# Kernel tuning notes

Measured on AMD Instinct MI355X. Metric: run time of the kernel, lower is better.

The kernel has to match this reference:

```python
import jax, jax.numpy as jnp
import numpy as np

B, M, E, H, A = 32, 512, 256, 8, 64


def setup_inputs() -> dict:
    key = jax.random.key(0)
    k0, k1, k2, k3, k4 = jax.random.split(key, 5)
    s = 1.0 / np.sqrt(E)
    x = jax.random.normal(k0, (B, M, E), dtype=jnp.float32)
    Wq = jax.random.normal(k1, (E, H * A), dtype=jnp.float32) * s
    Wk = jax.random.normal(k2, (E, H * A), dtype=jnp.float32) * s
    Wv = jax.random.normal(k3, (E, H * A), dtype=jnp.float32) * s
    Wr = jax.random.normal(k4, (E, A), dtype=jnp.float32) * s
    return {"x": x, "Wq": Wq, "Wk": Wk, "Wv": Wv, "Wr": Wr}


def reference(x, Wq, Wk, Wv, Wr):
    # Faithful to the original: (B, M, H*A) tensors are view()'d directly to
    # (H, B, M, A) / (H, B, A, M) without any transpose — this mixes batch
    # into the head axis exactly as the torch code does.
    q = (x @ Wq).reshape(H, B, M, A)   # query view
    k = (x @ Wk).reshape(H, B, A, M)   # keys viewed pre-transposed
    v = (x @ Wv).reshape(H, B, M, A)
    scores = jnp.einsum('hbma,hban->hbmn', q, k)      # (H, B, M, M)
    att = jax.nn.softmax(scores, axis=-1)
    out = jnp.einsum('hbmn,hbna->hbma', att, v)       # (H, B, M, A)
    out = out.mean(axis=0)                            # head-mean -> (B, M, A)
    return jax.nn.relu(out + x @ Wr)
```

## Files before the change

### kernel.cpp

```cpp
#include <hip/hip_runtime.h>
#include <math.h>


typedef _Float16 f16;
typedef _Float16 f16x2 __attribute__((ext_vector_type(2)));
typedef _Float16 f16x4 __attribute__((ext_vector_type(4)));
typedef _Float16 f16x8 __attribute__((ext_vector_type(8)));
typedef float    f32x4 __attribute__((ext_vector_type(4)));

typedef __attribute__((address_space(1))) const void* gas_t;
typedef __attribute__((address_space(3))) void* las_t;

__device__ __forceinline__ void gload16(const void* g, void* l) {
  __builtin_amdgcn_global_load_lds((gas_t)g, (las_t)l, 16, 0, 0);
}

__global__ __launch_bounds__(256) void k_cast(const float* __restrict__ in,
                                              f16* __restrict__ out, int n4) {
  int i = blockIdx.x * 256 + threadIdx.x;
  if (i < n4) {
    f32x4 v = reinterpret_cast<const f32x4*>(in)[i];
    f16x4 h;
    h[0] = (f16)v[0]; h[1] = (f16)v[1]; h[2] = (f16)v[2]; h[3] = (f16)v[3];
    reinterpret_cast<f16x4*>(out)[i] = h;
  }
}

__global__ __launch_bounds__(256) void k_transpose_w(const float* __restrict__ Wq,
                                                     const float* __restrict__ Wk,
                                                     const float* __restrict__ Wv,
                                                     const float* __restrict__ Wr,
                                                     f16* __restrict__ Wt,
                                                     f16* __restrict__ Wrt) {
  __shared__ f16 tile[64][68];
  int b = blockIdx.x;
  const float* src; f16* dst; int r0, c0, Cin;
  if (b < 96) {
    int ws = b >> 5, rem = b & 31;
    src = (ws == 0) ? Wq : (ws == 1) ? Wk : Wv;
    dst = Wt + ws * 512 * 256;
    Cin = 512; r0 = (rem >> 3) * 64; c0 = (rem & 7) * 64;
  } else {
    src = Wr; dst = Wrt; Cin = 64; r0 = (b - 96) * 64; c0 = 0;
  }
  int t = threadIdx.x;
#pragma unroll
  for (int u = 0; u < 8; ++u) {
    int e = u * 256 + t;
    int r = e >> 5, c = (e & 31) << 1;
    const float* p = src + (long)(r0 + r) * Cin + (c0 + c);
    f16x2 v; v[0] = (f16)p[0]; v[1] = (f16)p[1];
    *reinterpret_cast<f16x2*>(&tile[r][c]) = v;
  }
  __syncthreads();
#pragma unroll
  for (int u = 0; u < 16; ++u) {
    int f = u * 256 + t;
    int cc = f >> 6, rr = f & 63;
    dst[(long)(c0 + cc) * 256 + (r0 + rr)] = tile[rr][cc];
  }
}

template <int BN, bool F32OUT>
__global__ __launch_bounds__(256, 3) void k_gemm(const f16* __restrict__ Xh,
                                                 const f16* __restrict__ Wt,
                                                 f16* __restrict__ outH,
                                                 float* __restrict__ outF, int N) {
  __shared__ f16 Ash[128 * 64];
  __shared__ f16 Bsh[BN * 64];
  constexpr int NT = BN / 32;
  int t = threadIdx.x;
  int w = t >> 6, l = t & 63;
  int lrow = l & 15, lg = l >> 4;
  int wm = w >> 1, wn = w & 1;
  int rb = blockIdx.x * 128, cb = blockIdx.y * BN;

  f32x4 acc[4][NT] = {};

  for (int kt = 0; kt < 4; ++kt) {
    int kb = kt * 64;
    __syncthreads();
#pragma unroll
    for (int i = 0; i < 4; ++i) {
      int slot = i * 256 + t;
      int row = slot >> 3, pblk = slot & 7;
      int blk = pblk ^ (row & 7);
      gload16(Xh + (long)(rb + row) * 256 + kb + blk * 8, Ash + slot * 8);
    }
#pragma unroll
    for (int i = 0; i < BN / 32; ++i) {
      int slot = i * 256 + t;
      int row = slot >> 3, pblk = slot & 7;
      int blk = pblk ^ (row & 7);
      gload16(Wt + (long)(cb + row) * 256 + kb + blk * 8, Bsh + slot * 8);
    }
    __syncthreads();

    f16x8 af[4][2];
#pragma unroll
    for (int mi = 0; mi < 4; ++mi)
#pragma unroll
      for (int ks = 0; ks < 2; ++ks) {
        int r = 64 * wm + 16 * mi + lrow;
        af[mi][ks] = *reinterpret_cast<const f16x8*>(
            Ash + r * 64 + (((4 * ks + lg) ^ (lrow & 7)) * 8));
      }
#pragma unroll
    for (int nt = 0; nt < NT; ++nt) {
      int rB = (BN / 2) * wn + 16 * nt + lrow;
      f16x8 b0 = *reinterpret_cast<const f16x8*>(Bsh + rB * 64 + ((lg ^ (lrow & 7)) * 8));
      f16x8 b1 = *reinterpret_cast<const f16x8*>(Bsh + rB * 64 + (((4 + lg) ^ (lrow & 7)) * 8));
#pragma unroll
      for (int mi = 0; mi < 4; ++mi) {
        acc[mi][nt] = __builtin_amdgcn_mfma_f32_16x16x32_f16(af[mi][0], b0, acc[mi][nt], 0, 0, 0);
        acc[mi][nt] = __builtin_amdgcn_mfma_f32_16x16x32_f16(af[mi][1], b1, acc[mi][nt], 0, 0, 0);
      }
    }
  }
#pragma unroll
  for (int mi = 0; mi < 4; ++mi)
#pragma unroll
    for (int nt = 0; nt < NT; ++nt)
#pragma unroll
      for (int r = 0; r < 4; ++r) {
        int row = rb + 64 * wm + 16 * mi + 4 * (l >> 4) + r;
        int col = cb + (BN / 2) * wn + 16 * nt + lrow;
        float v = acc[mi][nt][r];
        if constexpr (F32OUT) {
          outF[(long)row * N + col] = v;
        } else {
          long idx = ((long)(col >> 9) << 23) + (long)row * 512 + (col & 511);
          outH[idx] = (f16)v;
        }
      }
}

__global__ __launch_bounds__(256, 4) void k_attn(const f16* __restrict__ Qh,
                                                 const f16* __restrict__ Kn,
                                                 const f16* __restrict__ Vn,
                                                 f16* __restrict__ Of) {
  __shared__ f16 Ksh[64 * 64];
  __shared__ f16 Vsh[64 * 64];
  __shared__ f16 Psh[4][32][72];
  int g = blockIdx.x, mb = blockIdx.y;
  int t = threadIdx.x, w = t >> 6, l = t & 63;
  int lrow = l & 15, lg = l >> 4, lk8 = lg * 8;
  long gp = (long)g * 32768;
  const f16* Qg = Qh + gp;
  const f16* Kg = Kn + gp;
  const f16* Vg = Vn + gp;
  f16* Og = Of + gp;
  int m0 = mb * 128 + w * 32;

  int sa = t >> 3;
  int so = (t & 7) * 8;

  f16x8 qf[2][2];
#pragma unroll
  for (int mi = 0; mi < 2; ++mi)
#pragma unroll
    for (int ks = 0; ks < 2; ++ks)
      qf[mi][ks] = *reinterpret_cast<const f16x8*>(Qg + (long)(m0 + 16 * mi + lrow) * 64 + 32 * ks + lk8);

  f32x4 accO[2][4] = {};
  float Mx[2] = {-INFINITY, -INFINITY}, Ls[2] = {0.f, 0.f};

  auto write_stage = [&](f16x8 kr0, f16x8 kr1, f16x8 vr0, f16x8 vr1) {
#pragma unroll
    for (int s = 0; s < 2; ++s) {
      f16x8 kr = s ? kr1 : kr0;
      int a = s * 32 + sa;
      int ab = a >> 3;
#pragma unroll
      for (int j = 0; j < 8; ++j) {
        int n = so + j;
        Ksh[n * 64 + ((ab ^ (n >> 3)) * 8) + (a & 7)] = kr[j];
      }
      f16x8 vr = s ? vr1 : vr0;
      int n2 = s * 32 + sa;
      int nb = n2 >> 3;
#pragma unroll
      for (int j = 0; j < 8; ++j) {
        int aa = so + j;
        Vsh[aa * 64 + ((nb ^ (aa >> 3)) * 8) + (n2 & 7)] = vr[j];
      }
    }
  };

  {
    f16x8 k0 = *reinterpret_cast<const f16x8*>(Kg + (long)(0 * 32 + sa) * 512 + so);
    f16x8 k1 = *reinterpret_cast<const f16x8*>(Kg + (long)(1 * 32 + sa) * 512 + so);
    f16x8 v0 = *reinterpret_cast<const f16x8*>(Vg + (long)(0 * 32 + sa) * 64 + so);
    f16x8 v1 = *reinterpret_cast<const f16x8*>(Vg + (long)(32 + sa) * 64 + so);
    write_stage(k0, k1, v0, v1);
  }
  __syncthreads();

  for (int c = 0; c < 8; ++c) {
    f16x8 kn0, kn1, vn0, vn1;
    if (c < 7) {
      int cn = c + 1;
      kn0 = *reinterpret_cast<const f16x8*>(Kg + (long)(0 * 32 + sa) * 512 + cn * 64 + so);
      kn1 = *reinterpret_cast<const f16x8*>(Kg + (long)(1 * 32 + sa) * 512 + cn * 64 + so);
      vn0 = *reinterpret_cast<const f16x8*>(Vg + (long)(cn * 64 + sa) * 64 + so);
      vn1 = *reinterpret_cast<const f16x8*>(Vg + (long)(cn * 64 + 32 + sa) * 64 + so);
    }

    f32x4 St[2][4] = {};
#pragma unroll
    for (int nt = 0; nt < 4; ++nt) {
      int n = 16 * nt + lrow, nb = n >> 3;
      f16x8 ka = *reinterpret_cast<const f16x8*>(Ksh + n * 64 + ((lg ^ nb) * 8));
      f16x8 kb = *reinterpret_cast<const f16x8*>(Ksh + n * 64 + (((4 + lg) ^ nb) * 8));
#pragma unroll
      for (int mi = 0; mi < 2; ++mi) {
        St[mi][nt] = __builtin_amdgcn_mfma_f32_16x16x32_f16(ka, qf[mi][0], St[mi][nt], 0, 0, 0);
        St[mi][nt] = __builtin_amdgcn_mfma_f32_16x16x32_f16(kb, qf[mi][1], St[mi][nt], 0, 0, 0);
      }
    }

    float scb[2][4];
#pragma unroll
    for (int mi = 0; mi < 2; ++mi) {
      float tm = St[mi][0][0];
#pragma unroll
      for (int nt = 0; nt < 4; ++nt)
#pragma unroll
        for (int r = 0; r < 4; ++r) tm = fmaxf(tm, St[mi][nt][r]);
      tm = fmaxf(tm, __shfl_xor(tm, 16));
      tm = fmaxf(tm, __shfl_xor(tm, 32));
      float nm = fmaxf(Mx[mi], tm);
      float sc = __expf(Mx[mi] - nm);
      Mx[mi] = nm;
      float ps = 0.f;
#pragma unroll
      for (int nt = 0; nt < 4; ++nt)
#pragma unroll
        for (int r = 0; r < 4; ++r) {
          float p = __expf(St[mi][nt][r] - nm);
          St[mi][nt][r] = p;
          ps += p;
        }
      ps += __shfl_xor(ps, 16);
      ps += __shfl_xor(ps, 32);
      Ls[mi] = Ls[mi] * sc + ps;
#pragma unroll
      for (int nt = 0; nt < 4; ++nt) {
        f16x4 p4;
        p4[0] = (f16)St[mi][nt][0]; p4[1] = (f16)St[mi][nt][1];
        p4[2] = (f16)St[mi][nt][2]; p4[3] = (f16)St[mi][nt][3];
        *reinterpret_cast<f16x4*>(&Psh[w][16 * mi + lrow][16 * nt + 4 * lg]) = p4;
      }
#pragma unroll
      for (int r = 0; r < 4; ++r) scb[mi][r] = __shfl(sc, 20 * lg + r);
    }
#pragma unroll
    for (int mi = 0; mi < 2; ++mi)
#pragma unroll
      for (int at = 0; at < 4; ++at)
#pragma unroll
        for (int r = 0; r < 4; ++r) accO[mi][at][r] *= scb[mi][r];

#pragma unroll
    for (int ks = 0; ks < 2; ++ks) {
      f16x8 pa[2];
#pragma unroll
      for (int mi = 0; mi < 2; ++mi)
        pa[mi] = *reinterpret_cast<const f16x8*>(&Psh[w][16 * mi + lrow][32 * ks + lk8]);
#pragma unroll
      for (int at = 0; at < 4; ++at) {
        int a = 16 * at + lrow, ab = a >> 3;
        f16x8 vb = *reinterpret_cast<const f16x8*>(Vsh + a * 64 + (((4 * ks + lg) ^ ab) * 8));
#pragma unroll
        for (int mi = 0; mi < 2; ++mi)
          accO[mi][at] = __builtin_amdgcn_mfma_f32_16x16x32_f16(pa[mi], vb, accO[mi][at], 0, 0, 0);
      }
    }

    __syncthreads();
    if (c < 7) write_stage(kn0, kn1, vn0, vn1);
    __syncthreads();
  }

#pragma unroll
  for (int mi = 0; mi < 2; ++mi) {
    float inv = 1.f / Ls[mi];
    float invb[4];
#pragma unroll
    for (int r = 0; r < 4; ++r) invb[r] = __shfl(inv, 20 * lg + r);
#pragma unroll
    for (int r = 0; r < 4; ++r) {
      int row = m0 + 16 * mi + 4 * lg + r;
#pragma unroll
      for (int at = 0; at < 4; ++at)
        Og[(long)row * 64 + 16 * at + lrow] = (f16)(accO[mi][at][r] * invb[r]);
    }
  }
}

__global__ __launch_bounds__(256) void k_finalize(const f16* __restrict__ Of,
                                                  const float* __restrict__ Rf,
                                                  float* __restrict__ out) {
  int i = blockIdx.x * 256 + threadIdx.x;
  f32x4 s = {};
#pragma unroll
  for (int h = 0; h < 8; ++h) {
    f16x4 o = reinterpret_cast<const f16x4*>(Of + (long)h * 1048576)[i];
#pragma unroll
    for (int j = 0; j < 4; ++j) s[j] += (float)o[j];
  }
  f32x4 r = reinterpret_cast<const f32x4*>(Rf)[i];
  f32x4 v = s * 0.125f + r;
#pragma unroll
  for (int j = 0; j < 4; ++j) v[j] = v[j] > 0.f ? v[j] : 0.f;
  reinterpret_cast<f32x4*>(out)[i] = v;
}

extern "C" void kernel_launch(void* const* d_in, const int* in_sizes, int n_in,
                              void* d_out, int out_size, void* d_ws, size_t ws_size,
                              hipStream_t stream) {
  const float* x  = (const float*)d_in[0];
  const float* Wq = (const float*)d_in[1];
  const float* Wk = (const float*)d_in[2];
  const float* Wv = (const float*)d_in[3];
  const float* Wr = (const float*)d_in[4];
  float* out = (float*)d_out;
  char* w = (char*)d_ws;

  f16*   Xh   = (f16*)(w + 0);
  f16*   Wt   = (f16*)(w + 8388608);
  f16*   Wrt  = (f16*)(w + 9175040);
  f16*   QKV  = (f16*)(w + 9207808);
  f16*   Qh   = QKV;
  f16*   Kn   = (f16*)(w + 25985024);
  f16*   Vn   = (f16*)(w + 42762240);
  float* Rf   = (float*)(w + 59539456);
  f16*   Of   = (f16*)(w + 63733760);

  k_cast<<<4096, 256, 0, stream>>>(x, Xh, 1048576);
  k_transpose_w<<<100, 256, 0, stream>>>(Wq, Wk, Wv, Wr, Wt, Wrt);

  k_gemm<128, false><<<dim3(128, 12), 256, 0, stream>>>(Xh, Wt, QKV, nullptr, 512);
  k_gemm<64, true><<<dim3(128, 1), 256, 0, stream>>>(Xh, Wrt, nullptr, Rf, 64);

  k_attn<<<dim3(256, 4), 256, 0, stream>>>(Qh, Kn, Vn, Of);
  k_finalize<<<1024, 256, 0, stream>>>(Of, Rf, out);
}
```

Before: 155.1 us.

## Pre-transpose K and V in global memory and drop LDS staging in attention

Two new transpose kernels rewrite K (64x512 per group) and V (512x64 per group) into transposed layouts ahead of attention. The attention kernel then reads MFMA operands straight from global memory and no longer uses LDS staging, the per-chunk barriers or the software prefetch. It also remaps block indices so the four row-blocks of a group run close together for L2 reuse, and raises wave priority around the MFMA sections. In exchange it adds two extra kernel launches and a full read and write of K and V, and the direct global loads may expose memory latency.

```diff
diff --git a/kernel.cpp b/kernel.cpp
--- a/kernel.cpp
+++ b/kernel.cpp
@@ -61,6 +61,31 @@
   }
 }
 
+__global__ __launch_bounds__(256) void k_transpose(const f16* __restrict__ in,
+                                                   f16* __restrict__ out,
+                                                   int R_, int C_) {
+  __shared__ f16 tile[64][68];
+  int g = blockIdx.x;
+  long gb = (long)g * R_ * C_;
+  int r0 = blockIdx.y * 64, c0 = blockIdx.z * 64;
+  int t = threadIdx.x;
+#pragma unroll
+  for (int u = 0; u < 8; ++u) {
+    int e = u * 256 + t;
+    int r = e >> 5, c = (e & 31) << 1;
+    const f16* p = in + gb + (long)(r0 + r) * C_ + (c0 + c);
+    f16x2 v; v[0] = p[0]; v[1] = p[1];
+    *reinterpret_cast<f16x2*>(&tile[r][c]) = v;
+  }
+  __syncthreads();
+#pragma unroll
+  for (int u = 0; u < 16; ++u) {
+    int f = u * 256 + t;
+    int cc = f >> 6, rr = f & 63;
+    out[gb + (long)(c0 + cc) * R_ + (r0 + rr)] = tile[rr][cc];
+  }
+}
+
 template <int BN, bool F32OUT>
 __global__ __launch_bounds__(256, 3) void k_gemm(const f16* __restrict__ Xh,
                                                  const f16* __restrict__ Wt,
@@ -136,25 +161,22 @@
 }
 
 __global__ __launch_bounds__(256, 4) void k_attn(const f16* __restrict__ Qh,
-                                                 const f16* __restrict__ Kn,
-                                                 const f16* __restrict__ Vn,
+                                                 const f16* __restrict__ Ktg,
+                                                 const f16* __restrict__ Vtg,
                                                  f16* __restrict__ Of) {
-  __shared__ f16 Ksh[64 * 64];
-  __shared__ f16 Vsh[64 * 64];
   __shared__ f16 Psh[4][32][72];
-  int g = blockIdx.x, mb = blockIdx.y;
+  int u = blockIdx.x;
+  int g = (u & 7) | ((u >> 5) << 3);
+  int mb = (u >> 3) & 3;
   int t = threadIdx.x, w = t >> 6, l = t & 63;
   int lrow = l & 15, lg = l >> 4, lk8 = lg * 8;
   long gp = (long)g * 32768;
   const f16* Qg = Qh + gp;
-  const f16* Kg = Kn + gp;
-  const f16* Vg = Vn + gp;
+  const f16* Kg = Ktg + gp;
+  const f16* Vg = Vtg + gp;
   f16* Og = Of + gp;
   int m0 = mb * 128 + w * 32;
 
-  int sa = t >> 3;
-  int so = (t & 7) * 8;
-
   f16x8 qf[2][2];
 #pragma unroll
   for (int mi = 0; mi < 2; ++mi)
@@ -165,59 +187,21 @@
   f32x4 accO[2][4] = {};
   float Mx[2] = {-INFINITY, -INFINITY}, Ls[2] = {0.f, 0.f};
 
-  auto write_stage = [&](f16x8 kr0, f16x8 kr1, f16x8 vr0, f16x8 vr1) {
-#pragma unroll
-    for (int s = 0; s < 2; ++s) {
-      f16x8 kr = s ? kr1 : kr0;
-      int a = s * 32 + sa;
-      int ab = a >> 3;
-#pragma unroll
-      for (int j = 0; j < 8; ++j) {
-        int n = so + j;
-        Ksh[n * 64 + ((ab ^ (n >> 3)) * 8) + (a & 7)] = kr[j];
-      }
-      f16x8 vr = s ? vr1 : vr0;
-      int n2 = s * 32 + sa;
-      int nb = n2 >> 3;
-#pragma unroll
-      for (int j = 0; j < 8; ++j) {
-        int aa = so + j;
-        Vsh[aa * 64 + ((nb ^ (aa >> 3)) * 8) + (n2 & 7)] = vr[j];
-      }
-    }
-  };
-
-  {
-    f16x8 k0 = *reinterpret_cast<const f16x8*>(Kg + (long)(0 * 32 + sa) * 512 + so);
-    f16x8 k1 = *reinterpret_cast<const f16x8*>(Kg + (long)(1 * 32 + sa) * 512 + so);
-    f16x8 v0 = *reinterpret_cast<const f16x8*>(Vg + (long)(0 * 32 + sa) * 64 + so);
-    f16x8 v1 = *reinterpret_cast<const f16x8*>(Vg + (long)(32 + sa) * 64 + so);
-    write_stage(k0, k1, v0, v1);
-  }
-  __syncthreads();
-
   for (int c = 0; c < 8; ++c) {
-    f16x8 kn0, kn1, vn0, vn1;
-    if (c < 7) {
-      int cn = c + 1;
-      kn0 = *reinterpret_cast<const f16x8*>(Kg + (long)(0 * 32 + sa) * 512 + cn * 64 + so);
-      kn1 = *reinterpret_cast<const f16x8*>(Kg + (long)(1 * 32 + sa) * 512 + cn * 64 + so);
-      vn0 = *reinterpret_cast<const f16x8*>(Vg + (long)(cn * 64 + sa) * 64 + so);
-      vn1 = *reinterpret_cast<const f16x8*>(Vg + (long)(cn * 64 + 32 + sa) * 64 + so);
-    }
-
     f32x4 St[2][4] = {};
+    __builtin_amdgcn_s_setprio(1);
 #pragma unroll
     for (int nt = 0; nt < 4; ++nt) {
-      int n = 16 * nt + lrow, nb = n >> 3;
-      f16x8 ka = *reinterpret_cast<const f16x8*>(Ksh + n * 64 + ((lg ^ nb) * 8));
-      f16x8 kb = *reinterpret_cast<const f16x8*>(Ksh + n * 64 + (((4 + lg) ^ nb) * 8));
+      const f16* kr = Kg + (long)(c * 64 + 16 * nt + lrow) * 64 + lk8;
+      f16x8 ka = *reinterpret_cast<const f16x8*>(kr);
+      f16x8 kb = *reinterpret_cast<const f16x8*>(kr + 32);
 #pragma unroll
       for (int mi = 0; mi < 2; ++mi) {
         St[mi][nt] = __builtin_amdgcn_mfma_f32_16x16x32_f16(ka, qf[mi][0], St[mi][nt], 0, 0, 0);
         St[mi][nt] = __builtin_amdgcn_mfma_f32_16x16x32_f16(kb, qf[mi][1], St[mi][nt], 0, 0, 0);
       }
     }
+    __builtin_amdgcn_s_setprio(0);
 
     float scb[2][4];
 #pragma unroll
@@ -261,6 +245,7 @@
 #pragma unroll
         for (int r = 0; r < 4; ++r) accO[mi][at][r] *= scb[mi][r];
 
+    __builtin_amdgcn_s_setprio(1);
 #pragma unroll
     for (int ks = 0; ks < 2; ++ks) {
       f16x8 pa[2];
@@ -269,17 +254,14 @@
         pa[mi] = *reinterpret_cast<const f16x8*>(&Psh[w][16 * mi + lrow][32 * ks + lk8]);
 #pragma unroll
       for (int at = 0; at < 4; ++at) {
-        int a = 16 * at + lrow, ab = a >> 3;
-        f16x8 vb = *reinterpret_cast<const f16x8*>(Vsh + a * 64 + (((4 * ks + lg) ^ ab) * 8));
+        f16x8 vb = *reinterpret_cast<const f16x8*>(
+            Vg + (long)(16 * at + lrow) * 512 + c * 64 + 32 * ks + lk8);
 #pragma unroll
         for (int mi = 0; mi < 2; ++mi)
           accO[mi][at] = __builtin_amdgcn_mfma_f32_16x16x32_f16(pa[mi], vb, accO[mi][at], 0, 0, 0);
       }
     }
-
-    __syncthreads();
-    if (c < 7) write_stage(kn0, kn1, vn0, vn1);
-    __syncthreads();
+    __builtin_amdgcn_s_setprio(0);
   }
 
 #pragma unroll
@@ -334,8 +316,10 @@
   f16*   Qh   = QKV;
   f16*   Kn   = (f16*)(w + 25985024);
   f16*   Vn   = (f16*)(w + 42762240);
-  float* Rf   = (float*)(w + 59539456);
-  f16*   Of   = (f16*)(w + 63733760);
+  f16*   Ktg  = (f16*)(w + 59539456);
+  f16*   Vtg  = (f16*)(w + 76316672);
+  float* Rf   = (float*)(w + 93093888);
+  f16*   Of   = (f16*)(w + 25985024);
 
   k_cast<<<4096, 256, 0, stream>>>(x, Xh, 1048576);
   k_transpose_w<<<100, 256, 0, stream>>>(Wq, Wk, Wv, Wr, Wt, Wrt);
@@ -343,6 +327,9 @@
   k_gemm<128, false><<<dim3(128, 12), 256, 0, stream>>>(Xh, Wt, QKV, nullptr, 512);
   k_gemm<64, true><<<dim3(128, 1), 256, 0, stream>>>(Xh, Wrt, nullptr, Rf, 64);
 
-  k_attn<<<dim3(256, 4), 256, 0, stream>>>(Qh, Kn, Vn, Of);
+  k_transpose<<<dim3(256, 1, 8), 256, 0, stream>>>(Kn, Ktg, 64, 512);
+  k_transpose<<<dim3(256, 8, 1), 256, 0, stream>>>(Vn, Vtg, 512, 64);
+
+  k_attn<<<1024, 256, 0, stream>>>(Qh, Ktg, Vtg, Of);
   k_finalize<<<1024, 256, 0, stream>>>(Of, Rf, out);
 }
```

Measured after the change: 183.3 us. 18.2% more time.
